# Optimization experiments

Hardware: AMD Instinct MI355X
Metric: run time of the kernel (lower is better)

The kernel has to match this reference:

```python
import jax, jax.numpy as jnp
import numpy as np

N_SIN = 3
BN_EPS = 1e-5

def kan(x, W1, W2, B1, B2):
    # x: [B, din]; W1: [din, dout, H, 1+2*n_sin]; W2: [din, dout, 1, H]
    # B1: [din, dout, H]; B2: [din, dout, 1]
    omega = (2.0 ** jnp.arange(N_SIN)).astype(x.dtype)          # [n_sin]
    ox = x[..., None] * omega                                   # [B, din, n_sin]
    feats = jnp.concatenate([x[..., None], jnp.sin(ox), jnp.cos(ox)], axis=-1)  # [B, din, F]
    h = jnp.einsum('bif,ijhf->bijh', feats, W1) + B1            # [B, din, dout, H]
    h = jax.nn.silu(h)
    out = jnp.einsum('bijh,ijh->bij', h, W2[:, :, 0, :]) + B2[:, :, 0]  # [B, din, dout]
    return out.sum(axis=1)                                      # [B, dout]

def setup_inputs() -> dict:
    key = jax.random.key(0)
    ks = jax.random.split(key, 20)
    B, DIN, DH, DOUT, H = 128, 128, 256, 128, 32
    F = 1 + 2 * N_SIN
    def n(k, shape, s=0.1):
        return jax.random.normal(k, shape, dtype=jnp.float32) * s
    return {
        'x': jax.random.normal(ks[0], (B, DIN), dtype=jnp.float32),
        'fc1_W1': n(ks[1], (DIN, DH, H, F)), 'fc1_W2': n(ks[2], (DIN, DH, 1, H)),
        'fc1_B1': n(ks[3], (DIN, DH, H)),    'fc1_B2': n(ks[4], (DIN, DH, 1)),
        'fc2_W1': n(ks[5], (DH, DOUT, H, F)), 'fc2_W2': n(ks[6], (DH, DOUT, 1, H)),
        'fc2_B1': n(ks[7], (DH, DOUT, H)),    'fc2_B2': n(ks[8], (DH, DOUT, 1)),
        'sk_W1': n(ks[9], (DIN, DOUT, H, F)), 'sk_W2': n(ks[10], (DIN, DOUT, 1, H)),
        'sk_B1': n(ks[11], (DIN, DOUT, H)),   'sk_B2': n(ks[12], (DIN, DOUT, 1)),
        'g1_w': n(ks[13], (DOUT, DOUT)), 'g1_b': n(ks[14], (DOUT,)),
        'g2_w': n(ks[15], (DOUT, DOUT)), 'g2_b': n(ks[16], (DOUT,)),
        'bn_w': jnp.ones((DOUT,), jnp.float32), 'bn_b': jnp.zeros((DOUT,), jnp.float32),
    }

def reference(x, fc1_W1, fc1_W2, fc1_B1, fc1_B2,
              fc2_W1, fc2_W2, fc2_B1, fc2_B2,
              sk_W1, sk_W2, sk_B1, sk_B2,
              g1_w, g1_b, g2_w, g2_b, bn_w, bn_b):
    residual = kan(x, sk_W1, sk_W2, sk_B1, sk_B2)                # [B, DOUT]
    h = kan(x, fc1_W1, fc1_W2, fc1_B1, fc1_B2)                   # [B, DH]
    h = jax.nn.elu(h)
    h = kan(h, fc2_W1, fc2_W2, fc2_B1, fc2_B2)                   # [B, DOUT]
    # dropout: eval-mode identity
    sig = jax.nn.sigmoid(h @ g1_w.T + g1_b)
    h = sig * (h @ g2_w.T + g2_b)                                # GLU gate
    h = h + residual
    mean = h.mean(axis=0)
    var = h.var(axis=0)                                          # biased, as torch BN
    h = (h - mean) * jax.lax.rsqrt(var + BN_EPS) * bn_w + bn_b
    return h
```

## Files before the change

### kernel.cpp

```cpp
#include <hip/hip_runtime.h>
#include <cstddef>
#include <cstdint>

#define BATCH 128
#define NF 7

typedef float v2f __attribute__((ext_vector_type(2)));

__device__ __forceinline__ v2f silu2(v2f a) {
    v2f t = a * -1.442695041f;
    v2f e;
    e.x = __builtin_amdgcn_exp2f(t.x);
    e.y = __builtin_amdgcn_exp2f(t.y);
    v2f d = e + 1.0f;
    v2f r;
    r.x = __builtin_amdgcn_rcpf(d.x);
    r.y = __builtin_amdgcn_rcpf(d.y);
    return a * r;
}

__global__ void feats_kernel(const float* __restrict__ in, float* __restrict__ out,
                             int din, int do_elu) {
    int t = blockIdx.x * blockDim.x + threadIdx.x;
    if (t >= din * BATCH) return;
    int b = t & (BATCH - 1);
    int i = t >> 7;
    float v = in[b * din + i];
    if (do_elu) v = (v > 0.0f) ? v : (__builtin_amdgcn_exp2f(v * 1.442695041f) - 1.0f);
    float s1, c1, s2, c2, s4, c4;
    sincosf(v, &s1, &c1);
    sincosf(2.0f * v, &s2, &c2);
    sincosf(4.0f * v, &s4, &c4);
    float* o = out + (size_t)i * (NF * 128) + (b & 63) * 2 + (b >> 6);
    o[0 * 128] = v;
    o[1 * 128] = s1;
    o[2 * 128] = s2;
    o[3 * 128] = s4;
    o[4 * 128] = c1;
    o[5 * 128] = c2;
    o[6 * 128] = c4;
}

template <int DIN, int DOUT, int CHUNK>
__global__ __launch_bounds__(256, 8) void kan_kernel(
    const float* __restrict__ fx,
    const float* __restrict__ W1,
    const float* __restrict__ W2,
    const float* __restrict__ B1,
    const float* __restrict__ B2,
    float* __restrict__ out)
{
    __shared__ float redbuf[4 * 128];
    const int j    = blockIdx.x;
    const int tid  = threadIdx.x;
    const int w    = tid >> 6;
    const int lane = tid & 63;
    const int i0   = blockIdx.y * CHUNK;

    v2f tot = (v2f)(0.0f);

    for (int t = 0; t < CHUNK / 4; ++t) {
        const int i = __builtin_amdgcn_readfirstlane(i0 + t * 4 + w);
        const size_t task = (size_t)i * DOUT + j;
        const float* __restrict__ w1p = W1 + task * 224;
        const float* __restrict__ b1p = B1 + task * 32;
        const float* __restrict__ w2p = W2 + task * 32;

        const float* fp = fx + (size_t)i * (NF * 128) + lane * 2;
        v2f f[NF];
        #pragma unroll
        for (int ff = 0; ff < NF; ++ff) f[ff] = *(const v2f*)(fp + ff * 128);

        v2f o = (v2f)(0.0f);
        #pragma unroll 1
        for (int hg = 0; hg < 4; ++hg) {
            #pragma unroll
            for (int hh = 0; hh < 8; ++hh) {
                const int h = hg * 8 + hh;
                const float* wr = w1p + h * 7;
                float b1v = b1p[h];
                float w2v = w2p[h];
                v2f a = {b1v, b1v};
                #pragma unroll
                for (int ff = 0; ff < NF; ++ff) {
                    float wv = wr[ff];
                    a.x = fmaf(f[ff].x, wv, a.x);
                    a.y = fmaf(f[ff].y, wv, a.y);
                }
                v2f s = silu2(a);
                o.x = fmaf(s.x, w2v, o.x);
                o.y = fmaf(s.y, w2v, o.y);
            }
        }
        float b2v = B2[task];
        tot += o + b2v;
    }

    redbuf[w * 128 + lane]      = tot.x;
    redbuf[w * 128 + 64 + lane] = tot.y;
    __syncthreads();
    if (tid < 128) {
        float s = redbuf[tid] + redbuf[128 + tid] + redbuf[256 + tid] + redbuf[384 + tid];
        atomicAdd(&out[(size_t)tid * DOUT + j], s);
    }
}

__device__ __forceinline__ int shidx(int k, int b) { return (k << 7) + ((b + k) & 127); }

__global__ __launch_bounds__(128) void glu_bn_kernel(
    const float* __restrict__ h2,
    const float* __restrict__ resid,
    const float* __restrict__ g1w, const float* __restrict__ g1b,
    const float* __restrict__ g2w, const float* __restrict__ g2b,
    const float* __restrict__ bnw, const float* __restrict__ bnb,
    float* __restrict__ out)
{
    __shared__ float sh[128 * 128];
    const int j   = blockIdx.x;
    const int tid = threadIdx.x;

    for (int b2 = 0; b2 < 128; ++b2)
        sh[shidx(tid, b2)] = h2[(size_t)b2 * 128 + tid];
    __syncthreads();

    const float* g1r = g1w + (size_t)j * 128;
    const float* g2r = g2w + (size_t)j * 128;
    float d1 = g1b[j], d2 = g2b[j];
    for (int k = 0; k < 128; ++k) {
        float hv = sh[shidx(k, tid)];
        d1 = fmaf(hv, g1r[k], d1);
        d2 = fmaf(hv, g2r[k], d2);
    }
    float sg = __builtin_amdgcn_rcpf(1.0f + __builtin_amdgcn_exp2f(d1 * -1.442695041f));
    float v  = sg * d2 + resid[(size_t)tid * 128 + j];

    float s = v, ss = v * v;
    #pragma unroll
    for (int m = 1; m < 64; m <<= 1) {
        s  += __shfl_xor(s,  m, 64);
        ss += __shfl_xor(ss, m, 64);
    }
    __syncthreads();
    if ((tid & 63) == 0) { sh[(tid >> 6) * 2] = s; sh[(tid >> 6) * 2 + 1] = ss; }
    __syncthreads();
    s  = sh[0] + sh[2];
    ss = sh[1] + sh[3];
    float mean = s * (1.0f / 128.0f);
    float var  = ss * (1.0f / 128.0f) - mean * mean;
    out[(size_t)tid * 128 + j] = (v - mean) * rsqrtf(var + 1e-5f) * bnw[j] + bnb[j];
}

extern "C" void kernel_launch(void* const* d_in, const int* in_sizes, int n_in,
                              void* d_out, int out_size, void* d_ws, size_t ws_size,
                              hipStream_t stream) {
    const float* x      = (const float*)d_in[0];
    const float* fc1_W1 = (const float*)d_in[1];
    const float* fc1_W2 = (const float*)d_in[2];
    const float* fc1_B1 = (const float*)d_in[3];
    const float* fc1_B2 = (const float*)d_in[4];
    const float* fc2_W1 = (const float*)d_in[5];
    const float* fc2_W2 = (const float*)d_in[6];
    const float* fc2_B1 = (const float*)d_in[7];
    const float* fc2_B2 = (const float*)d_in[8];
    const float* sk_W1  = (const float*)d_in[9];
    const float* sk_W2  = (const float*)d_in[10];
    const float* sk_B1  = (const float*)d_in[11];
    const float* sk_B2  = (const float*)d_in[12];
    const float* g1w    = (const float*)d_in[13];
    const float* g1b    = (const float*)d_in[14];
    const float* g2w    = (const float*)d_in[15];
    const float* g2b    = (const float*)d_in[16];
    const float* bnw    = (const float*)d_in[17];
    const float* bnb    = (const float*)d_in[18];
    float* out = (float*)d_out;

    float* ws    = (float*)d_ws;
    float* h1    = ws;
    float* h2    = h1 + 128 * 256;
    float* resid = h2 + 128 * 128;
    float* fx    = resid + 128 * 128;
    float* fh    = fx + 128 * NF * 128;

    hipMemsetAsync(h1, 0, (size_t)(128 * 256 + 2 * 128 * 128) * sizeof(float), stream);

    feats_kernel<<<dim3((128 * BATCH) / 256), 256, 0, stream>>>(x, fx, 128, 0);

    kan_kernel<128, 256, 16><<<dim3(256, 8), 256, 0, stream>>>(
        fx, fc1_W1, fc1_W2, fc1_B1, fc1_B2, h1);
    kan_kernel<128, 128, 8><<<dim3(128, 16), 256, 0, stream>>>(
        fx, sk_W1, sk_W2, sk_B1, sk_B2, resid);

    feats_kernel<<<dim3((256 * BATCH) / 256), 256, 0, stream>>>(h1, fh, 256, 1);

    kan_kernel<256, 128, 16><<<dim3(128, 16), 256, 0, stream>>>(
        fh, fc2_W1, fc2_W2, fc2_B1, fc2_B2, h2);

    glu_bn_kernel<<<dim3(128), 128, 0, stream>>>(
        h2, resid, g1w, g1b, g2w, g2b, bnw, bnb, out);
}
```

Measured before the change: 153.5 us.

## Software-pipeline KAN weight and feature loads with double buffering

```diff
diff --git a/kernel.cpp b/kernel.cpp
--- a/kernel.cpp
+++ b/kernel.cpp
@@ -41,6 +41,57 @@
     o[6 * 128] = c4;
 }
 
+
+#define LOAD_GRP(W, g) do {                                                    \
+    _Pragma("unroll")                                                          \
+    for (int q = 0; q < 7; ++q)                                                \
+        *(float4*)&W[q * 4] = *(const float4*)(w1p + (g) * 28 + q * 4);        \
+    *(float4*)&W[28] = *(const float4*)(b1p + (g) * 4);                        \
+    *(float4*)&W[32] = *(const float4*)(w2p + (g) * 4);                        \
+} while (0)
+
+#define COMP_GRP(W, fbuf) do {                                                 \
+    _Pragma("unroll")                                                          \
+    for (int hh = 0; hh < 4; ++hh) {                                           \
+        v2f a = { W[28 + hh], W[28 + hh] };                                    \
+        _Pragma("unroll")                                                      \
+        for (int ff = 0; ff < NF; ++ff) {                                      \
+            float wv = W[hh * 7 + ff];                                         \
+            a.x = fmaf(fbuf[ff].x, wv, a.x);                                   \
+            a.y = fmaf(fbuf[ff].y, wv, a.y);                                   \
+        }                                                                      \
+        v2f s = silu2(a);                                                      \
+        o.x = fmaf(s.x, W[32 + hh], o.x);                                      \
+        o.y = fmaf(s.y, W[32 + hh], o.y);                                      \
+    }                                                                          \
+} while (0)
+
+#define TASK_BODY(tt, fcur, fnxt, PREF) do {                                   \
+    const int i_ = __builtin_amdgcn_readfirstlane(i0 + (tt) * 4 + w);          \
+    const size_t task_ = (size_t)i_ * DOUT + j;                                \
+    const float* __restrict__ w1p = W1 + task_ * 224;                          \
+    const float* __restrict__ b1p = B1 + task_ * 32;                           \
+    const float* __restrict__ w2p = W2 + task_ * 32;                           \
+    float WA[36], WB[36];                                                      \
+    LOAD_GRP(WA, 0);                                                           \
+    if (PREF) {                                                                \
+        const int i2_ = __builtin_amdgcn_readfirstlane(i0 + ((tt) + 1) * 4 + w);\
+        const float* fp2 = fx + (size_t)i2_ * (NF * 128) + lane * 2;           \
+        _Pragma("unroll")                                                      \
+        for (int ff = 0; ff < NF; ++ff) fnxt[ff] = *(const v2f*)(fp2 + ff * 128);\
+    }                                                                          \
+    v2f o = (v2f)(0.0f);                                                       \
+    _Pragma("unroll 1")                                                        \
+    for (int g = 0; g < 8; g += 2) {                                           \
+        LOAD_GRP(WB, g + 1);                                                   \
+        COMP_GRP(WA, fcur);                                                    \
+        if (g + 2 < 8) LOAD_GRP(WA, g + 2);                                    \
+        COMP_GRP(WB, fcur);                                                    \
+    }                                                                          \
+    float b2v = B2[task_];                                                     \
+    tot += o + b2v;                                                            \
+} while (0)
+
 template <int DIN, int DOUT, int CHUNK>
 __global__ __launch_bounds__(256, 8) void kan_kernel(
     const float* __restrict__ fx,
@@ -58,42 +109,19 @@
     const int i0   = blockIdx.y * CHUNK;
 
     v2f tot = (v2f)(0.0f);
-
-    for (int t = 0; t < CHUNK / 4; ++t) {
-        const int i = __builtin_amdgcn_readfirstlane(i0 + t * 4 + w);
-        const size_t task = (size_t)i * DOUT + j;
-        const float* __restrict__ w1p = W1 + task * 224;
-        const float* __restrict__ b1p = B1 + task * 32;
-        const float* __restrict__ w2p = W2 + task * 32;
-
-        const float* fp = fx + (size_t)i * (NF * 128) + lane * 2;
-        v2f f[NF];
+    v2f fA[NF], fB[NF];
+
+    {
+        const int ip = __builtin_amdgcn_readfirstlane(i0 + w);
+        const float* fp = fx + (size_t)ip * (NF * 128) + lane * 2;
         #pragma unroll
-        for (int ff = 0; ff < NF; ++ff) f[ff] = *(const v2f*)(fp + ff * 128);
-
-        v2f o = (v2f)(0.0f);
-        #pragma unroll 1
-        for (int hg = 0; hg < 4; ++hg) {
-            #pragma unroll
-            for (int hh = 0; hh < 8; ++hh) {
-                const int h = hg * 8 + hh;
-                const float* wr = w1p + h * 7;
-                float b1v = b1p[h];
-                float w2v = w2p[h];
-                v2f a = {b1v, b1v};
-                #pragma unroll
-                for (int ff = 0; ff < NF; ++ff) {
-                    float wv = wr[ff];
-                    a.x = fmaf(f[ff].x, wv, a.x);
-                    a.y = fmaf(f[ff].y, wv, a.y);
-                }
-                v2f s = silu2(a);
-                o.x = fmaf(s.x, w2v, o.x);
-                o.y = fmaf(s.y, w2v, o.y);
-            }
-        }
-        float b2v = B2[task];
-        tot += o + b2v;
+        for (int ff = 0; ff < NF; ++ff) fA[ff] = *(const v2f*)(fp + ff * 128);
+    }
+
+    #pragma unroll
+    for (int t = 0; t < CHUNK / 4; t += 2) {
+        TASK_BODY(t,     fA, fB, true);
+        TASK_BODY(t + 1, fB, fA, (t + 2 < CHUNK / 4));
     }
 
     redbuf[w * 128 + lane]      = tot.x;
```

After: 232.1 us. +51.2%, slower.
